# Kernel optimization log

Hardware: AMD Instinct MI355X
Metric: run time of the kernel (lower is better)

The kernel has to match this reference:

```python
import jax, jax.numpy as jnp
import numpy as np

SR = 44100
WT_LEN = 512
N_WT = 20
B, T = 16, 262144


def setup_inputs() -> dict:
    key = jax.random.key(0)
    k1, k2, k3, k4 = jax.random.split(key, 4)
    # realistic fundamental frequencies in [50, 500) Hz
    pitch = 50.0 + 450.0 * jax.random.uniform(k1, (B, T, 1), dtype=jnp.float32)
    amplitude = jax.random.uniform(k2, (B, T, 1), dtype=jnp.float32)
    attention = jax.random.uniform(k3, (B, T, N_WT), dtype=jnp.float32)
    # learned wavetables [N_WT, WT_LEN]; first 4 are fixed sine cycles, rest learnable noise
    i = np.arange(WT_LEN, dtype=np.float32)
    sines = np.stack([np.sin((c + 1) * 2 * np.pi * i / WT_LEN) for c in range(4)]).astype(np.float32)
    rest = 0.01 * np.asarray(jax.random.normal(k4, (N_WT - 4, WT_LEN)), dtype=np.float32)
    wt = np.concatenate([sines, rest], axis=0)
    # module enforces wt[-1] == wt[0] (periodic closure)
    wt[:, -1] = wt[:, 0]
    return {"pitch": pitch, "amplitude": amplitude, "attention": attention,
            "wavetables": jnp.asarray(wt)}


def reference(pitch, amplitude, attention, wavetables):
    L = wavetables.shape[1]
    # tanh applied to learnable tables only (indices >= 4)
    wt = jnp.concatenate([wavetables[:4], jnp.tanh(wavetables[4:])], axis=0)  # [K, L]
    freq = pitch[..., 0]                                   # [B, T]
    increment = freq / SR * L                              # [B, T]
    index = jnp.cumsum(increment, axis=-1) - increment[:, :1]
    index = index % L
    idx_low = jnp.floor(index)
    idx_high = jnp.ceil(index)
    alpha = index - idx_low                                # [B, T]
    il = idx_low.astype(jnp.int32)
    ih = (idx_high.astype(jnp.int32)) % L
    wt_t = wt.T                                            # [L, K]
    low = wt_t[il]                                         # [B, T, K] single gather for all tables
    high = wt_t[ih]                                        # [B, T, K]
    waveforms = low + alpha[..., None] * (high - low)      # [B, T, K]
    mixed = jnp.sum(waveforms * attention, axis=-1)        # [B, T]
    return (mixed[..., None] * amplitude)                  # [B, T, 1]
```

## Files before the change

kernel.cpp:

```cpp
#include <hip/hip_runtime.h>
#include <math.h>

#define WT_LEN 512
#define N_WT 20
#define B_ 16
#define T_ 262144
#define TOTAL (B_ * T_)
#define CHUNK 8192
#define NCHR 32
#define NCH  512

__device__ __forceinline__ float to_inc1(float x) {
    return (x / 44100.0f) * 512.0f;
}
__device__ __forceinline__ float4 to_inc4(float4 p) {
    float4 r;
    r.x = to_inc1(p.x); r.y = to_inc1(p.y);
    r.z = to_inc1(p.z); r.w = to_inc1(p.w);
    return r;
}

__global__ __launch_bounds__(1024) void up_kernel(
        const float* __restrict__ pitch, float* __restrict__ A13) {
    __shared__ float red[2048];
    const int t = threadIdx.x;
    const size_t g0 = (size_t)blockIdx.x * CHUNK;

    const float4* p4 = (const float4*)(pitch + g0);
    float4 v0 = to_inc4(p4[2 * t]);
    float4 v1 = to_inc4(p4[2 * t + 1]);
    float t0 = v0.x + v0.y, t1 = v0.z + v0.w;
    float t2 = v1.x + v1.y, t3 = v1.z + v1.w;
    red[t] = (t0 + t1) + (t2 + t3);
    __syncthreads();
    int off_prev = 0, off = 1024;
    for (int sz = 512; sz >= 1; sz >>= 1) {
        if (t < sz) red[off + t] = red[off_prev + 2 * t] + red[off_prev + 2 * t + 1];
        __syncthreads();
        off_prev = off; off += sz;
    }
    if (t == 0) A13[blockIdx.x] = red[2046];
}

__global__ __launch_bounds__(1024) void mid_kernel(
        const float* __restrict__ A13, const float* __restrict__ pitch,
        const float* __restrict__ wtg, float* __restrict__ S13,
        float* __restrict__ X0, float* __restrict__ WTT) {
    int r = threadIdx.x;
    if (r < B_) {
        float l0[32], l1[16], l2[8], l3[4], l4[2], l5;
        for (int i = 0; i < 32; ++i) l0[i] = A13[r * 32 + i];
        for (int i = 0; i < 16; ++i) l1[i] = l0[2 * i] + l0[2 * i + 1];
        for (int i = 0; i < 8;  ++i) l2[i] = l1[2 * i] + l1[2 * i + 1];
        for (int i = 0; i < 4;  ++i) l3[i] = l2[2 * i] + l2[2 * i + 1];
        for (int i = 0; i < 2;  ++i) l4[i] = l3[2 * i] + l3[2 * i + 1];
        l5 = l4[0] + l4[1];

        float s4[2], s3[4], s2[8], s1[16], s0[32];
        s4[0] = l4[0]; s4[1] = l5;
        s3[0] = l3[0];
        for (int i = 0; i < 2; ++i) {
            s3[2 * i + 1] = s4[i];
            if (2 * i + 2 < 4) s3[2 * i + 2] = s4[i] + l3[2 * i + 2];
        }
        s2[0] = l2[0];
        for (int i = 0; i < 4; ++i) {
            s2[2 * i + 1] = s3[i];
            if (2 * i + 2 < 8) s2[2 * i + 2] = s3[i] + l2[2 * i + 2];
        }
        s1[0] = l1[0];
        for (int i = 0; i < 8; ++i) {
            s1[2 * i + 1] = s2[i];
            if (2 * i + 2 < 16) s1[2 * i + 2] = s2[i] + l1[2 * i + 2];
        }
        s0[0] = l0[0];
        for (int i = 0; i < 16; ++i) {
            s0[2 * i + 1] = s1[i];
            if (2 * i + 2 < 32) s0[2 * i + 2] = s1[i] + l0[2 * i + 2];
        }
        for (int i = 0; i < 32; ++i) S13[r * 32 + i] = s0[i];
        X0[r] = to_inc1(pitch[(size_t)r * T_]);
    }
    for (int e = threadIdx.x; e < WT_LEN * N_WT; e += 1024) {
        int c = e / WT_LEN;
        int i = e - c * WT_LEN;
        float v = wtg[e];
        if (c >= 4) v = tanhf(v);
        WTT[i * N_WT + c] = v;
    }
}

__global__ __launch_bounds__(1024) void down_kernel(
        const float* __restrict__ pitch, const float* __restrict__ S13,
        float* __restrict__ sout) {
    __shared__ float a[2048];
    const int t = threadIdx.x;
    const int c = blockIdx.x;
    const size_t g0 = (size_t)c * CHUNK;

    const float4* p4 = (const float4*)(pitch + g0);
    float4 va = to_inc4(p4[2 * t]);
    float4 vb = to_inc4(p4[2 * t + 1]);
    float x0 = va.x, x2 = va.z, x4 = vb.x, x6 = vb.z;
    float t0 = va.x + va.y, t1 = va.z + va.w;
    float t2 = vb.x + vb.y, t3 = vb.z + vb.w;
    float u0 = t0 + t1, u1 = t2 + t3;
    a[t] = u0 + u1;
    __syncthreads();

    int bp = 0, b = 1024;
    for (int sz = 512; sz >= 2; sz >>= 1) {
        if (t < sz) a[b + t] = a[bp + 2 * t] + a[bp + 2 * t + 1];
        __syncthreads();
        bp = b; b += sz;
    }

    const float P   = (c & (NCHR - 1)) ? S13[c - 1] : 0.0f;
    const float T13 = S13[c];
    if (t == 0) {
        a[2044] = P + a[2044];
        a[2045] = T13;
    }
    __syncthreads();

    const int offk[10] = {0, 1024, 1536, 1792, 1920, 1984, 2016, 2032, 2040, 2044};
    for (int k = 11; k >= 3; --k) {
        int m = 1 << (13 - k), half = m >> 1;
        int bk = offk[k - 3], bn = offk[k - 2];
        if (t < half) {
            float sn = a[bn + t];
            int j = 2 * t + 2;
            float av = (j < m) ? a[bk + j] : 0.0f;
            a[bk + 2 * t + 1] = sn;
            if (j < m) a[bk + j] = sn + av;
        }
        if (t == 0) a[bk] = P + a[bk];
        __syncthreads();
    }

    float S3prev = t ? a[t - 1] : P;
    float s3t = a[t];
    float s1a = S3prev + t0;
    float s2a = S3prev + u0;
    float s1c = s2a + t2;
    (void)t1; (void)t3; (void)u1;

    float4* q4 = (float4*)(sout + g0);
    q4[2 * t]     = make_float4(S3prev + x0, s1a, s1a + x2, s2a);
    q4[2 * t + 1] = make_float4(s2a + x4, s1c, s1c + x6, s3t);
}

__global__ __launch_bounds__(512) void mix_kernel(
        float* io, const float* __restrict__ X0,
        const float* __restrict__ amp, const float* __restrict__ att,
        const float* __restrict__ WTT, int ntiles) {
    __shared__ float wt_lds[WT_LEN * N_WT];
    {
        const float4* src = (const float4*)WTT;
        float4* dst = (float4*)wt_lds;
#pragma unroll
        for (int r = 0; r < 5; ++r)
            dst[threadIdx.x + 512 * r] = src[threadIdx.x + 512 * r];
    }
    __syncthreads();

    for (int tile = blockIdx.x; tile < ntiles; tile += gridDim.x) {
        int gid = tile * 512 + threadIdx.x;
        int row = gid >> 18;
        float S = io[gid];
        float y = S - X0[row];

        float qf  = floorf(y * (1.0f / 512.0f));
        float idx = fmaf(-512.0f, qf, y);
        if (idx < 0.0f)    idx += 512.0f;
        if (idx >= 512.0f) idx -= 512.0f;

        float fl0   = floorf(idx);
        float alpha = idx - fl0;
        int il = ((int)fl0) & (WT_LEN - 1);
        int ih = (il + (alpha > 0.0f ? 1 : 0)) & (WT_LEN - 1);

        const float4* lo4 = (const float4*)(&wt_lds[il * N_WT]);
        const float4* hi4 = (const float4*)(&wt_lds[ih * N_WT]);
        const float4* a4  = (const float4*)(att + (size_t)gid * N_WT);

        float acc = 0.0f;
#pragma unroll
        for (int v = 0; v < 5; ++v) {
            float4 lo = lo4[v];
            float4 hi = hi4[v];
            float4 at = a4[v];
            acc += at.x * (lo.x + alpha * (hi.x - lo.x));
            acc += at.y * (lo.y + alpha * (hi.y - lo.y));
            acc += at.z * (lo.z + alpha * (hi.z - lo.z));
            acc += at.w * (lo.w + alpha * (hi.w - lo.w));
        }
        io[gid] = acc * amp[gid];
    }
}

extern "C" void kernel_launch(void* const* d_in, const int* in_sizes, int n_in,
                              void* d_out, int out_size, void* d_ws, size_t ws_size,
                              hipStream_t stream) {
    const float* pitch = (const float*)d_in[0];
    const float* amp   = (const float*)d_in[1];
    const float* att   = (const float*)d_in[2];
    const float* wtg   = (const float*)d_in[3];
    float* S = (float*)d_out;

    float* A13 = (float*)d_ws;
    float* S13 = A13 + NCH;
    float* X0  = S13 + NCH;
    float* WTT = X0 + 64;

    up_kernel<<<NCH, 1024, 0, stream>>>(pitch, A13);
    mid_kernel<<<1, 1024, 0, stream>>>(A13, pitch, wtg, S13, X0, WTT);
    down_kernel<<<NCH, 1024, 0, stream>>>(pitch, S13, S);
    mix_kernel<<<1024, 512, 0, stream>>>(S, X0, amp, att, WTT,
                                         TOTAL / 512);
}
```

Before: 500.7 us.

## Fuse scan down-sweep with wavetable mixing into a single kernel

Merges the down-sweep prefix-sum kernel and the wavetable mixing kernel so each thread computes phases for its 8 samples and immediately interpolates and mixes them. This removes the intermediate phase array's global write and re-read and one kernel launch. In exchange, each thread reads a contiguous 640-byte span of attention, giving strided, less coalesced loads. LDS use per block grows, and only 512 large blocks carry the dominant memory stream.

```diff
diff --git a/kernel.cpp b/kernel.cpp
--- a/kernel.cpp
+++ b/kernel.cpp
@@ -90,13 +90,24 @@
     }
 }
 
-__global__ __launch_bounds__(1024) void down_kernel(
+__global__ __launch_bounds__(1024) void downmix_kernel(
         const float* __restrict__ pitch, const float* __restrict__ S13,
-        float* __restrict__ sout) {
+        const float* __restrict__ X0v, const float* __restrict__ amp,
+        const float* __restrict__ att, const float* __restrict__ WTT,
+        float* __restrict__ out) {
     __shared__ float a[2048];
+    __shared__ float wt_lds[WT_LEN * N_WT];
     const int t = threadIdx.x;
     const int c = blockIdx.x;
     const size_t g0 = (size_t)c * CHUNK;
+
+    {
+        const float4* src = (const float4*)WTT;
+        float4* dst = (float4*)wt_lds;
+        dst[t]        = src[t];
+        dst[t + 1024] = src[t + 1024];
+        if (t < 512) dst[t + 2048] = src[t + 2048];
+    }
 
     const float4* p4 = (const float4*)(pitch + g0);
     float4 va = to_inc4(p4[2 * t]);
@@ -145,30 +156,20 @@
     float s1c = s2a + t2;
     (void)t1; (void)t3; (void)u1;
 
-    float4* q4 = (float4*)(sout + g0);
-    q4[2 * t]     = make_float4(S3prev + x0, s1a, s1a + x2, s2a);
-    q4[2 * t + 1] = make_float4(s2a + x4, s1c, s1c + x6, s3t);
-}
-
-__global__ __launch_bounds__(512) void mix_kernel(
-        float* io, const float* __restrict__ X0,
-        const float* __restrict__ amp, const float* __restrict__ att,
-        const float* __restrict__ WTT, int ntiles) {
-    __shared__ float wt_lds[WT_LEN * N_WT];
-    {
-        const float4* src = (const float4*)WTT;
-        float4* dst = (float4*)wt_lds;
+    float Sv[8] = { S3prev + x0, s1a, s1a + x2, s2a,
+                    s2a + x4,    s1c, s1c + x6, s3t };
+
+    const float x0row = X0v[c >> 5];
+    const float4* a4  = (const float4*)(att + (size_t)(g0 + 8 * (size_t)t) * N_WT);
+    const float4* am4 = (const float4*)(amp + g0);
+    float4 am0 = am4[2 * t];
+    float4 am1 = am4[2 * t + 1];
+    float ampv[8] = {am0.x, am0.y, am0.z, am0.w, am1.x, am1.y, am1.z, am1.w};
+
+    float res[8];
 #pragma unroll
-        for (int r = 0; r < 5; ++r)
-            dst[threadIdx.x + 512 * r] = src[threadIdx.x + 512 * r];
-    }
-    __syncthreads();
-
-    for (int tile = blockIdx.x; tile < ntiles; tile += gridDim.x) {
-        int gid = tile * 512 + threadIdx.x;
-        int row = gid >> 18;
-        float S = io[gid];
-        float y = S - X0[row];
+    for (int j = 0; j < 8; ++j) {
+        float y = Sv[j] - x0row;
 
         float qf  = floorf(y * (1.0f / 512.0f));
         float idx = fmaf(-512.0f, qf, y);
@@ -182,21 +183,24 @@
 
         const float4* lo4 = (const float4*)(&wt_lds[il * N_WT]);
         const float4* hi4 = (const float4*)(&wt_lds[ih * N_WT]);
-        const float4* a4  = (const float4*)(att + (size_t)gid * N_WT);
 
         float acc = 0.0f;
 #pragma unroll
         for (int v = 0; v < 5; ++v) {
             float4 lo = lo4[v];
             float4 hi = hi4[v];
-            float4 at = a4[v];
+            float4 at = a4[5 * j + v];
             acc += at.x * (lo.x + alpha * (hi.x - lo.x));
             acc += at.y * (lo.y + alpha * (hi.y - lo.y));
             acc += at.z * (lo.z + alpha * (hi.z - lo.z));
             acc += at.w * (lo.w + alpha * (hi.w - lo.w));
         }
-        io[gid] = acc * amp[gid];
-    }
+        res[j] = acc * ampv[j];
+    }
+
+    float4* q4 = (float4*)(out + g0);
+    q4[2 * t]     = make_float4(res[0], res[1], res[2], res[3]);
+    q4[2 * t + 1] = make_float4(res[4], res[5], res[6], res[7]);
 }
 
 extern "C" void kernel_launch(void* const* d_in, const int* in_sizes, int n_in,
@@ -206,7 +210,6 @@
     const float* amp   = (const float*)d_in[1];
     const float* att   = (const float*)d_in[2];
     const float* wtg   = (const float*)d_in[3];
-    float* S = (float*)d_out;
 
     float* A13 = (float*)d_ws;
     float* S13 = A13 + NCH;
@@ -215,7 +218,6 @@
 
     up_kernel<<<NCH, 1024, 0, stream>>>(pitch, A13);
     mid_kernel<<<1, 1024, 0, stream>>>(A13, pitch, wtg, S13, X0, WTT);
-    down_kernel<<<NCH, 1024, 0, stream>>>(pitch, S13, S);
-    mix_kernel<<<1024, 512, 0, stream>>>(S, X0, amp, att, WTT,
-                                         TOTAL / 512);
-}
+    downmix_kernel<<<NCH, 1024, 0, stream>>>(pitch, S13, X0, amp, att, WTT,
+                                             (float*)d_out);
+}
```

Result: slower. 540.9 us (+8.0%).

## Eliminate mid kernel by folding chunk-prefix and wavetable prep into neighbors

Applied to the files above, without the earlier changes.

Removes the single-block mid_kernel. In down_kernel, thread 0 now recomputes each chunk's scan prefix directly from the per-chunk totals, using the same pairwise tree so the results stay bit-identical. Each mix_kernel block now applies tanh, transposes the wavetables into LDS itself and computes the per-row starting increment. The cumulative sum goes to workspace instead of the output buffer. This saves one launch and a serialized one-block kernel, at the cost of redundant tanh work in every mix block and a longer serial prologue in down_kernel thread 0.

```diff
diff --git a/kernel.cpp b/kernel.cpp
--- a/kernel.cpp
+++ b/kernel.cpp
@@ -42,61 +42,52 @@
     if (t == 0) A13[blockIdx.x] = red[2046];
 }
 
-__global__ __launch_bounds__(1024) void mid_kernel(
-        const float* __restrict__ A13, const float* __restrict__ pitch,
-        const float* __restrict__ wtg, float* __restrict__ S13,
-        float* __restrict__ X0, float* __restrict__ WTT) {
-    int r = threadIdx.x;
-    if (r < B_) {
-        float l0[32], l1[16], l2[8], l3[4], l4[2], l5;
-        for (int i = 0; i < 32; ++i) l0[i] = A13[r * 32 + i];
-        for (int i = 0; i < 16; ++i) l1[i] = l0[2 * i] + l0[2 * i + 1];
-        for (int i = 0; i < 8;  ++i) l2[i] = l1[2 * i] + l1[2 * i + 1];
-        for (int i = 0; i < 4;  ++i) l3[i] = l2[2 * i] + l2[2 * i + 1];
-        for (int i = 0; i < 2;  ++i) l4[i] = l3[2 * i] + l3[2 * i + 1];
-        l5 = l4[0] + l4[1];
-
-        float s4[2], s3[4], s2[8], s1[16], s0[32];
-        s4[0] = l4[0]; s4[1] = l5;
-        s3[0] = l3[0];
-        for (int i = 0; i < 2; ++i) {
-            s3[2 * i + 1] = s4[i];
-            if (2 * i + 2 < 4) s3[2 * i + 2] = s4[i] + l3[2 * i + 2];
-        }
-        s2[0] = l2[0];
-        for (int i = 0; i < 4; ++i) {
-            s2[2 * i + 1] = s3[i];
-            if (2 * i + 2 < 8) s2[2 * i + 2] = s3[i] + l2[2 * i + 2];
-        }
-        s1[0] = l1[0];
-        for (int i = 0; i < 8; ++i) {
-            s1[2 * i + 1] = s2[i];
-            if (2 * i + 2 < 16) s1[2 * i + 2] = s2[i] + l1[2 * i + 2];
-        }
-        s0[0] = l0[0];
-        for (int i = 0; i < 16; ++i) {
-            s0[2 * i + 1] = s1[i];
-            if (2 * i + 2 < 32) s0[2 * i + 2] = s1[i] + l0[2 * i + 2];
-        }
-        for (int i = 0; i < 32; ++i) S13[r * 32 + i] = s0[i];
-        X0[r] = to_inc1(pitch[(size_t)r * T_]);
-    }
-    for (int e = threadIdx.x; e < WT_LEN * N_WT; e += 1024) {
-        int c = e / WT_LEN;
-        int i = e - c * WT_LEN;
-        float v = wtg[e];
-        if (c >= 4) v = tanhf(v);
-        WTT[i * N_WT + c] = v;
-    }
-}
-
-__global__ __launch_bounds__(1024) void down_kernel(
-        const float* __restrict__ pitch, const float* __restrict__ S13,
+__device__ __forceinline__ float l1f(const float* A, int m) { return A[2*m] + A[2*m+1]; }
+__device__ __forceinline__ float l2f(const float* A, int m) { return l1f(A,2*m) + l1f(A,2*m+1); }
+__device__ __forceinline__ float l3f(const float* A, int m) { return l2f(A,2*m) + l2f(A,2*m+1); }
+__device__ __forceinline__ float l4f(const float* A, int m) { return l3f(A,2*m) + l3f(A,2*m+1); }
+
+__device__ float s0_of(const float* __restrict__ A, int j) {
+    if (j == 0) return A[0];
+    float p0 = 0.f, p1 = 0.f, p2 = 0.f, p3 = 0.f;
+    bool h0 = false, h1 = false, h2 = false, h3 = false;
+    float base;
+    int m = j;
+    if ((m & 1) == 0) { p0 = A[m]; h0 = true; m = (m - 2) >> 1; }
+    else m >>= 1;
+    if (m == 0) { base = l1f(A, 0); goto comb; }
+    if ((m & 1) == 0) { p1 = l1f(A, m); h1 = true; m = (m - 2) >> 1; }
+    else m >>= 1;
+    if (m == 0) { base = l2f(A, 0); goto comb; }
+    if ((m & 1) == 0) { p2 = l2f(A, m); h2 = true; m = (m - 2) >> 1; }
+    else m >>= 1;
+    if (m == 0) { base = l3f(A, 0); goto comb; }
+    if ((m & 1) == 0) { p3 = l3f(A, m); h3 = true; m = (m - 2) >> 1; }
+    else m >>= 1;
+    base = (m == 0) ? l4f(A, 0) : (l4f(A, 0) + l4f(A, 1));
+comb:
+    if (h3) base += p3;
+    if (h2) base += p2;
+    if (h1) base += p1;
+    if (h0) base += p0;
+    return base;
+}
+
+__global__ __launch_bounds__(1024, 8) void down_kernel(
+        const float* __restrict__ pitch, const float* __restrict__ A13,
         float* __restrict__ sout) {
     __shared__ float a[2048];
     const int t = threadIdx.x;
     const int c = blockIdx.x;
     const size_t g0 = (size_t)c * CHUNK;
+
+    float P = 0.0f, T13 = 0.0f;
+    if (t == 0) {
+        const float* A = A13 + ((c >> 5) << 5);
+        const int lc = c & (NCHR - 1);
+        if (lc) P = s0_of(A, lc - 1);
+        T13 = s0_of(A, lc);
+    }
 
     const float4* p4 = (const float4*)(pitch + g0);
     float4 va = to_inc4(p4[2 * t]);
@@ -115,8 +106,6 @@
         bp = b; b += sz;
     }
 
-    const float P   = (c & (NCHR - 1)) ? S13[c - 1] : 0.0f;
-    const float T13 = S13[c];
     if (t == 0) {
         a[2044] = P + a[2044];
         a[2045] = T13;
@@ -151,24 +140,27 @@
 }
 
 __global__ __launch_bounds__(512) void mix_kernel(
-        float* io, const float* __restrict__ X0,
+        const float* __restrict__ Sbuf, const float* __restrict__ pitch,
         const float* __restrict__ amp, const float* __restrict__ att,
-        const float* __restrict__ WTT, int ntiles) {
+        const float* __restrict__ wtg, float* __restrict__ out, int ntiles) {
     __shared__ float wt_lds[WT_LEN * N_WT];
-    {
-        const float4* src = (const float4*)WTT;
-        float4* dst = (float4*)wt_lds;
-#pragma unroll
-        for (int r = 0; r < 5; ++r)
-            dst[threadIdx.x + 512 * r] = src[threadIdx.x + 512 * r];
-    }
+    __shared__ float x0s[B_];
+    for (int e = threadIdx.x; e < WT_LEN * N_WT; e += 512) {
+        int c = e >> 9;
+        int i = e & (WT_LEN - 1);
+        float v = wtg[e];
+        if (c >= 4) v = tanhf(v);
+        wt_lds[i * N_WT + c] = v;
+    }
+    if (threadIdx.x < B_)
+        x0s[threadIdx.x] = to_inc1(pitch[(size_t)threadIdx.x << 18]);
     __syncthreads();
 
     for (int tile = blockIdx.x; tile < ntiles; tile += gridDim.x) {
         int gid = tile * 512 + threadIdx.x;
         int row = gid >> 18;
-        float S = io[gid];
-        float y = S - X0[row];
+        float S = Sbuf[gid];
+        float y = S - x0s[row];
 
         float qf  = floorf(y * (1.0f / 512.0f));
         float idx = fmaf(-512.0f, qf, y);
@@ -195,7 +187,7 @@
             acc += at.z * (lo.z + alpha * (hi.z - lo.z));
             acc += at.w * (lo.w + alpha * (hi.w - lo.w));
         }
-        io[gid] = acc * amp[gid];
+        out[gid] = acc * amp[gid];
     }
 }
 
@@ -206,16 +198,12 @@
     const float* amp   = (const float*)d_in[1];
     const float* att   = (const float*)d_in[2];
     const float* wtg   = (const float*)d_in[3];
-    float* S = (float*)d_out;
 
     float* A13 = (float*)d_ws;
-    float* S13 = A13 + NCH;
-    float* X0  = S13 + NCH;
-    float* WTT = X0 + 64;
+    float* S   = A13 + 1024;
 
     up_kernel<<<NCH, 1024, 0, stream>>>(pitch, A13);
-    mid_kernel<<<1, 1024, 0, stream>>>(A13, pitch, wtg, S13, X0, WTT);
-    down_kernel<<<NCH, 1024, 0, stream>>>(pitch, S13, S);
-    mix_kernel<<<1024, 512, 0, stream>>>(S, X0, amp, att, WTT,
-                                         TOTAL / 512);
-}
+    down_kernel<<<NCH, 1024, 0, stream>>>(pitch, A13, S);
+    mix_kernel<<<1024, 512, 0, stream>>>(S, pitch, amp, att, wtg,
+                                         (float*)d_out, TOTAL / 512);
+}
```

Result: faster. 485.1 us (-3.1%).
